# Optimization experiments

Measured on AMD Instinct MI355X. Metric: run time of the kernel, lower is better.

## Reference

```python
import jax, jax.numpy as jnp
import numpy as np

DIM = 128      # input node feature dim
GS = 64        # SAGEConv output dim
AF = 32        # additional (ir_score) feature dim
NB = 2         # nb_classes
G = 8192       # num_graphs in batch
NPG = 16       # nodes per graph
N = G * NPG    # total nodes = 131072
E = 2097152    # total edges (avg degree 16)


def setup_inputs() -> dict:
    key = jax.random.key(0)
    ks = jax.random.split(key, 10)

    def w(k, shape, fan_in):
        return jax.random.normal(k, shape, jnp.float32) / np.sqrt(fan_in)

    return {
        "x": jax.random.normal(ks[0], (N, DIM), jnp.float32),
        "edge_index": jax.random.randint(ks[1], (2, E), 0, N),
        "set_indices": jax.random.randint(ks[2], (G, 2), 0, NPG),
        "batch_ids": jnp.repeat(jnp.arange(G), NPG),  # sorted graph ids, PyG style
        "ir_score": jax.random.uniform(ks[3], (G, AF), jnp.float32),
        "W_l": w(ks[4], (DIM, GS), DIM),
        "b_l": jnp.zeros((GS,), jnp.float32),
        "W_r": w(ks[5], (DIM, GS), DIM),
        "W_ir": w(ks[6], (AF, 2 * GS), AF),
        "b_ir": jnp.zeros((2 * GS,), jnp.float32),
        "W1": w(ks[7], ((2 * GS) * (2 * GS), 200), (2 * GS) * (2 * GS)),
        "b1": jnp.zeros((200,), jnp.float32),
        "W2": w(ks[8], (200, NB), 200),
        "b2": jnp.zeros((NB,), jnp.float32),
    }


def reference(x, edge_index, set_indices, batch_ids, ir_score,
              W_l, b_l, W_r, W_ir, b_ir, W1, b1, W2, b2):
    n = x.shape[0]
    src, dst = edge_index[0], edge_index[1]

    # SAGEConv (mean aggregation): out = lin_l(mean_{j in N(i)} x_j) + lin_r(x_i)
    agg = jax.ops.segment_sum(x[src], dst, num_segments=n)           # [N, DIM]
    deg = jax.ops.segment_sum(jnp.ones((src.shape[0],), x.dtype), dst, num_segments=n)
    mean = agg / jnp.maximum(deg, 1.0)[:, None]
    h = jax.nn.relu(mean @ W_l + b_l + x @ W_r)                      # [N, GS]

    # per-graph node counts -> index bases (cumsum), then global pair indices
    g = set_indices.shape[0]
    num_nodes = jax.ops.segment_sum(jnp.ones((n,), jnp.float32), batch_ids, num_segments=g)
    csum = jnp.cumsum(num_nodes.astype(jnp.int64))
    index_bases = jnp.concatenate([jnp.zeros((1,), jnp.int64), csum[:-1]])
    sib = index_bases[:, None] + set_indices                         # [G, 2]

    pair = h[sib].reshape(g, 2 * GS)                                 # gather + flatten

    # fusion: relu(linear(ir_score)) then per-graph outer product
    S = jax.nn.relu(ir_score @ W_ir + b_ir)                          # [G, 2*GS]
    outer = jnp.einsum('gi,gj->gij', pair, S).reshape(g, -1)         # [G, (2GS)^2]

    # decode MLP
    z = jax.nn.relu(outer @ W1 + b1)                                 # [G, 200]
    logits = z @ W2 + b2                                             # [G, NB]
    return logits
```

## Files before the change

kernel.cpp:

```cpp
#include <hip/hip_runtime.h>

#define NN   131072
#define GG   8192
#define EE   2097152
#define KBIG 16384
#define NPAD 224
#define NSPLIT 8
#define NSEL  16384
#define SBUCK 256
#define SUBC  4
#define SCAPS 336
#define SCAPT (SUBC*SCAPS)

typedef _Float16 half_t;
typedef __attribute__((ext_vector_type(8))) _Float16 half8;
typedef __attribute__((ext_vector_type(4))) float floatx4;

__device__ inline floatx4 mfma16(half8 a, half8 b, floatx4 c) {
  return __builtin_amdgcn_mfma_f32_16x16x32_f16(a, b, c, 0, 0, 0);
}

__global__ void prep_w(const float* __restrict__ Wl, const float* __restrict__ Wr,
                       half_t* __restrict__ Wt) {
  int idx = blockIdx.x * blockDim.x + threadIdx.x;
  int n = idx >> 7, k = idx & 127;
  float v = (n < 64) ? Wl[k * 64 + n] : Wr[k * 64 + (n - 64)];
  Wt[n * 128 + k] = (half_t)v;
}
__global__ void prep_w1p(const float* __restrict__ W1, half_t* __restrict__ W1p) {
  int idx = blockIdx.x * blockDim.x + threadIdx.x;
  int lane = idx & 63;
  int t = idx >> 6;
  int nt = t % 14; t /= 14;
  int jc = t & 3;  t >>= 2;
  int i  = t & 15; t >>= 4;
  int split = t;
  int n = nt * 16 + (lane & 15);
  int k0 = split * 2048 + i * 128 + jc * 32 + (lane >> 4) * 8;
  half8 v;
#pragma unroll
  for (int e = 0; e < 8; e++)
    v[e] = (half_t)((n < 200) ? W1[(size_t)(k0 + e) * 200 + n] : 0.f);
  *(half8*)(W1p + (size_t)idx * 8) = v;
}

__global__ void set_slots(const int* __restrict__ set_idx, int* __restrict__ nodemap,
                          int* __restrict__ slot_node) {
  int idx = blockIdx.x * blockDim.x + threadIdx.x;
  int g = idx >> 1, which = idx & 1;
  int node = g * 16 + set_idx[g * 2 + which];
  slot_node[idx] = node;
  nodemap[node] = idx;
}

__global__ void filter_scatter(const int* __restrict__ src, const int* __restrict__ dst,
                               const int* __restrict__ nodemap,
                               int* __restrict__ scnt, unsigned int* __restrict__ sbuf) {
  int e = blockIdx.x * blockDim.x + threadIdx.x;
  int d = dst[e];
  int slot = nodemap[d];
  if (slot >= 0) {
    int b = slot >> 6;
    int sub = blockIdx.x & (SUBC - 1);
    int pos = atomicAdd(&scnt[(b * SUBC + sub) * 16], 1);
    if (pos < SCAPS)
      sbuf[(size_t)(b * SUBC + sub) * SCAPS + pos] =
          (unsigned int)src[e] | ((unsigned int)(slot & 63) << 17);
  }
}

__global__ __launch_bounds__(256) void y_gemm(const float* __restrict__ x,
                                              const half_t* __restrict__ WtG,
                                              half_t* __restrict__ y16) {
  __shared__ half_t wlds[64 * 128];
  __shared__ half_t ybuf[64 * 72];
  int tid = threadIdx.x, w = tid >> 6, lane = tid & 63;
  int m = lane & 15, q = lane >> 4, kc = q * 8;
#pragma unroll
  for (int it = 0; it < 4; it++) {
    int cb = (it * 4 + w) * 64;
    const half_t* g = WtG + ((size_t)cb + lane) * 8;
    half_t* l = wlds + (size_t)cb * 8;
    __builtin_amdgcn_global_load_lds((const __attribute__((address_space(1))) uint32_t*)g,
                                     (__attribute__((address_space(3))) uint32_t*)l, 16, 0, 0);
  }
  int node0 = blockIdx.x * 64 + w * 16;
  float4 xu[4][2];
#pragma unroll
  for (int step = 0; step < 4; step++) {
    const float* xp = x + (size_t)(node0 + m) * 128 + step * 32 + kc;
    xu[step][0] = *(const float4*)xp;
    xu[step][1] = *(const float4*)(xp + 4);
  }
  __syncthreads();
  floatx4 acc[4];
#pragma unroll
  for (int nt = 0; nt < 4; nt++) acc[nt] = (floatx4){0.f, 0.f, 0.f, 0.f};
#pragma unroll
  for (int step = 0; step < 4; step++) {
    float4 u0 = xu[step][0], u1 = xu[step][1];
    half8 av = {(half_t)u0.x, (half_t)u0.y, (half_t)u0.z, (half_t)u0.w,
                (half_t)u1.x, (half_t)u1.y, (half_t)u1.z, (half_t)u1.w};
    int k0 = step * 32 + kc;
#pragma unroll
    for (int nt = 0; nt < 4; nt++) {
      half8 bv = *(const half8*)(wlds + (nt * 16 + m) * 128 + k0);
      acc[nt] = mfma16(av, bv, acc[nt]);
    }
  }
#pragma unroll
  for (int nt = 0; nt < 4; nt++)
#pragma unroll
    for (int r = 0; r < 4; r++)
      ybuf[(w * 16 + q * 4 + r) * 72 + nt * 16 + m] = (half_t)acc[nt][r];
  __syncthreads();
#pragma unroll
  for (int c = tid; c < 512; c += 256) {
    int row = c >> 3, co = (c & 7) * 8;
    *(half8*)(y16 + (size_t)(blockIdx.x * 64 + row) * 64 + co) =
        *(const half8*)(ybuf + row * 72 + co);
  }
}

__global__ __launch_bounds__(256) void r_slots(const float* __restrict__ x,
                                               const half_t* __restrict__ WtG,
                                               const float* __restrict__ b_l,
                                               const int* __restrict__ slot_node,
                                               half_t* __restrict__ r_slot) {
  int tid = threadIdx.x, w = tid >> 6, lane = tid & 63;
  int m = lane & 15, q = lane >> 4, kc = q * 8;
  int s0 = blockIdx.x * 64 + w * 16;
  int node = slot_node[s0 + m];
  floatx4 acc[4];
#pragma unroll
  for (int nt = 0; nt < 4; nt++) acc[nt] = (floatx4){0.f, 0.f, 0.f, 0.f};
#pragma unroll
  for (int step = 0; step < 4; step++) {
    int k0 = step * 32 + kc;
    const float* xp = x + (size_t)node * 128 + k0;
    float4 u0 = *(const float4*)xp;
    float4 u1 = *(const float4*)(xp + 4);
    half8 av = {(half_t)u0.x, (half_t)u0.y, (half_t)u0.z, (half_t)u0.w,
                (half_t)u1.x, (half_t)u1.y, (half_t)u1.z, (half_t)u1.w};
#pragma unroll
    for (int nt = 0; nt < 4; nt++) {
      half8 bv = *(const half8*)(WtG + (size_t)(64 + nt * 16 + m) * 128 + k0);
      acc[nt] = mfma16(av, bv, acc[nt]);
    }
  }
#pragma unroll
  for (int nt = 0; nt < 4; nt++) {
    int n = nt * 16 + m;
    float bias = b_l[n];
#pragma unroll
    for (int r = 0; r < 4; r++) {
      int s = s0 + q * 4 + r;
      r_slot[(size_t)s * 64 + n] = (half_t)(acc[nt][r] + bias);
    }
  }
}

__global__ __launch_bounds__(256) void slot_agg(const unsigned int* __restrict__ sbuf,
                                                const int* __restrict__ scnt,
                                                const half_t* __restrict__ y16,
                                                const half_t* __restrict__ r_slot,
                                                half_t* __restrict__ h_slot) {
  __shared__ int sorted[SCAPT];
  __shared__ int hist[64];
  __shared__ int base[64];
  __shared__ int start[65];
  int b = blockIdx.x, tid = threadIdx.x;
  if (tid < 64) hist[tid] = 0;
  __syncthreads();
  unsigned int myedge[2 * SUBC];
  int mycnt = 0;
#pragma unroll
  for (int sub = 0; sub < SUBC; sub++) {
    int n = scnt[(b * SUBC + sub) * 16]; if (n > SCAPS) n = SCAPS;
    const unsigned int* eb = sbuf + (size_t)(b * SUBC + sub) * SCAPS;
    for (int e = tid; e < n; e += 256) {
      unsigned int pk = eb[e];
      myedge[mycnt++] = pk;
      atomicAdd(&hist[pk >> 17], 1);
    }
  }
  __syncthreads();
  if (tid < 64) {
    int v = hist[tid];
    int sum = v;
#pragma unroll
    for (int off = 1; off < 64; off <<= 1) {
      int u = __shfl_up(sum, off);
      if (tid >= off) sum += u;
    }
    start[tid] = sum - v;
    base[tid]  = sum - v;
    if (tid == 63) start[64] = sum;
  }
  __syncthreads();
  for (int i = 0; i < mycnt; i++) {
    unsigned int pk = myedge[i];
    int pos = atomicAdd(&base[pk >> 17], 1);
    sorted[pos] = (int)(pk & 0x1FFFF);
  }
  __syncthreads();
  int s = tid >> 2, p = tid & 3;
  int e0 = start[s], e1 = start[s + 1];
  float acc[16];
#pragma unroll
  for (int j = 0; j < 16; j++) acc[j] = 0.f;
  int e = e0;
  for (; e + 2 <= e1; e += 2) {
    int s0 = sorted[e], s1 = sorted[e + 1];
    const half8* p0 = (const half8*)(y16 + (size_t)s0 * 64 + p * 16);
    const half8* p1 = (const half8*)(y16 + (size_t)s1 * 64 + p * 16);
    half8 a0 = p0[0], c0 = p0[1], a1 = p1[0], c1 = p1[1];
#pragma unroll
    for (int j = 0; j < 8; j++) {
      acc[j]     += (float)a0[j] + (float)a1[j];
      acc[8 + j] += (float)c0[j] + (float)c1[j];
    }
  }
  if (e < e1) {
    int s0 = sorted[e];
    const half8* p0 = (const half8*)(y16 + (size_t)s0 * 64 + p * 16);
    half8 a0 = p0[0], c0 = p0[1];
#pragma unroll
    for (int j = 0; j < 8; j++) { acc[j] += (float)a0[j]; acc[8 + j] += (float)c0[j]; }
  }
  int slot = b * 64 + s;
  float inv = 1.0f / fmaxf((float)(e1 - e0), 1.0f);
  const half8* rr = (const half8*)(r_slot + (size_t)slot * 64 + p * 16);
  half8 r0 = rr[0], r1 = rr[1];
  half8 o0, o1;
#pragma unroll
  for (int j = 0; j < 8; j++) {
    o0[j] = (half_t)fmaxf(acc[j] * inv + (float)r0[j], 0.f);
    o1[j] = (half_t)fmaxf(acc[8 + j] * inv + (float)r1[j], 0.f);
  }
  half8* hp = (half8*)(h_slot + (size_t)slot * 64 + p * 16);
  hp[0] = o0;
  hp[1] = o1;
}

__global__ void s_pair_kernel(const float* __restrict__ ir, const float* __restrict__ W_ir,
                              const float* __restrict__ b_ir, half_t* __restrict__ S16,
                              const half_t* __restrict__ h_slot,
                              const int* __restrict__ nodemap,
                              const int* __restrict__ set_idx, half_t* __restrict__ pair16) {
  int idx = blockIdx.x * blockDim.x + threadIdx.x;
  int g = idx >> 7, o = idx & 127;
  const float* irow = ir + g * 32;
  float sv = b_ir[o];
#pragma unroll
  for (int a = 0; a < 32; a++) sv += irow[a] * W_ir[a * 128 + o];
  S16[idx] = (half_t)fmaxf(sv, 0.f);
  int which = o >> 6, c = o & 63;
  int node = g * 16 + set_idx[g * 2 + which];
  int slot = nodemap[node];
  pair16[idx] = h_slot[(size_t)slot * 64 + c];
}

__global__ __launch_bounds__(256, 2) void biggemm(const half_t* __restrict__ pair16,
                                                  const half_t* __restrict__ S16,
                                                  const half_t* __restrict__ W1p,
                                                  float* __restrict__ zpart) {
  __shared__ __align__(16) half_t bbuf[2][28 * 512];
  __shared__ half_t pls[16][128];
  int bx = blockIdx.x;
  int mt = bx >> 3, split = bx & 7;
  int g0 = mt * 128;
  int tid = threadIdx.x, w = tid >> 6, lane = tid & 63;
  int wm = w >> 1, wn = w & 1;
  int m = lane & 15, q = lane >> 4, kc = q * 8;
  int ntb = wn * 7;

  auto stage = [&](int ii, int halfsel, int bufsel) {
#pragma unroll
    for (int ff = 0; ff < 7; ff++) {
      int f = ff * 4 + w;
      const half_t* gsrc = W1p + (((size_t)(split * 16 + ii) * 56) + halfsel * 28 + f) * 512 + lane * 8;
      half_t* ldst = &bbuf[bufsel][f * 512];
      __builtin_amdgcn_global_load_lds((const __attribute__((address_space(1))) uint32_t*)gsrc,
                                       (__attribute__((address_space(3))) uint32_t*)ldst, 16, 0, 0);
    }
  };

  stage(0, 0, 0);

  {
    int row = tid & 127, sel = tid >> 7;
    half8 pa = *(const half8*)(pair16 + (size_t)(g0 + row) * 128 + split * 16 + sel * 8);
#pragma unroll
    for (int j = 0; j < 8; j++) pls[sel * 8 + j][row] = pa[j];
  }

  half8 sf[4][4];
#pragma unroll
  for (int sub = 0; sub < 4; sub++) {
    int grow = g0 + wm * 64 + sub * 16 + m;
#pragma unroll
    for (int jc = 0; jc < 4; jc++)
      sf[sub][jc] = *(const half8*)(S16 + (size_t)grow * 128 + jc * 32 + kc);
  }

  floatx4 acc[4][7];
#pragma unroll
  for (int sb = 0; sb < 4; sb++)
#pragma unroll
    for (int t = 0; t < 7; t++) acc[sb][t] = (floatx4){0.f, 0.f, 0.f, 0.f};

  for (int i = 0; i < 16; i++) {
    half_t p0, p1, p2, p3;
#pragma unroll
    for (int h2 = 0; h2 < 2; h2++) {
      __syncthreads();
      if (h2 == 0) {
        p0 = pls[i][wm * 64 + 0 * 16 + m];
        p1 = pls[i][wm * 64 + 1 * 16 + m];
        p2 = pls[i][wm * 64 + 2 * 16 + m];
        p3 = pls[i][wm * 64 + 3 * 16 + m];
        stage(i, 1, 1);
      } else if (i < 15) {
        stage(i + 1, 0, 0);
      }
      const half_t* bb = bbuf[h2];
#pragma unroll
      for (int jj = 0; jj < 2; jj++) {
        const int jc = h2 * 2 + jj;
        half8 a0 = sf[0][jc] * p0;
        half8 a1 = sf[1][jc] * p1;
        half8 a2 = sf[2][jc] * p2;
        half8 a3 = sf[3][jc] * p3;
#pragma unroll
        for (int t = 0; t < 7; t++) {
          half8 bv = *(const half8*)(bb + (jj * 14 + ntb + t) * 512 + lane * 8);
          acc[0][t] = mfma16(a0, bv, acc[0][t]);
          acc[1][t] = mfma16(a1, bv, acc[1][t]);
          acc[2][t] = mfma16(a2, bv, acc[2][t]);
          acc[3][t] = mfma16(a3, bv, acc[3][t]);
        }
      }
    }
  }

  float* ebuf = (float*)bbuf;
#pragma unroll
  for (int c = 0; c < 4; c++) {
    __syncthreads();
    if (wm == (c >> 1)) {
      int sb0 = (c & 1) * 2;
#pragma unroll
      for (int ss = 0; ss < 2; ss++) {
#pragma unroll
        for (int t = 0; t < 7; t++)
#pragma unroll
          for (int r = 0; r < 4; r++) {
            int lr = ss * 16 + q * 4 + r;
            ebuf[lr * 228 + (ntb + t) * 16 + m] = acc[sb0 + ss][t][r];
          }
      }
    }
    __syncthreads();
    int rbase = g0 + (c >> 1) * 64 + (c & 1) * 32;
#pragma unroll
    for (int u = tid; u < 1792; u += 256) {
      int lr = u / 56, co = (u % 56) * 4;
      *(float4*)(zpart + ((size_t)split * GG + rbase + lr) * NPAD + co) =
          *(const float4*)(ebuf + lr * 228 + co);
    }
  }
}

__global__ __launch_bounds__(256) void reduce_mlp(const float* __restrict__ zpart,
                                                  const float* __restrict__ b1,
                                                  const float* __restrict__ W2,
                                                  const float* __restrict__ b2,
                                                  float* __restrict__ out) {
  int tid = threadIdx.x;
  int w = tid >> 6, lane = tid & 63;
  int g = blockIdx.x * 4 + w;
  float p0 = 0.f, p1 = 0.f;
#pragma unroll
  for (int qq = 0; qq < 4; qq++) {
    int c = qq * 64 + lane;
    if (c < 200) {
      float z = 0.f;
#pragma unroll
      for (int sp = 0; sp < NSPLIT; sp++)
        z += zpart[((size_t)sp * GG + g) * NPAD + c];
      z += b1[c];
      z = fmaxf(z, 0.f);
      p0 += z * W2[c * 2];
      p1 += z * W2[c * 2 + 1];
    }
  }
#pragma unroll
  for (int off = 32; off; off >>= 1) {
    p0 += __shfl_down(p0, off);
    p1 += __shfl_down(p1, off);
  }
  if (lane == 0) {
    out[g * 2] = p0 + b2[0];
    out[g * 2 + 1] = p1 + b2[1];
  }
}

extern "C" void kernel_launch(void* const* d_in, const int* in_sizes, int n_in,
                              void* d_out, int out_size, void* d_ws, size_t ws_size,
                              hipStream_t stream) {
  const float* x     = (const float*)d_in[0];
  const int*   ei    = (const int*)d_in[1];
  const int*   setix = (const int*)d_in[2];
  const float* ir    = (const float*)d_in[4];
  const float* W_l   = (const float*)d_in[5];
  const float* b_l   = (const float*)d_in[6];
  const float* W_r   = (const float*)d_in[7];
  const float* W_ir  = (const float*)d_in[8];
  const float* b_ir  = (const float*)d_in[9];
  const float* W1    = (const float*)d_in[10];
  const float* b1    = (const float*)d_in[11];
  const float* W2    = (const float*)d_in[12];
  const float* b2    = (const float*)d_in[13];
  float* out = (float*)d_out;

  char* ws = (char*)d_ws;
  size_t off = 0;
  auto alloc = [&](size_t bytes) -> void* {
    void* p = ws + off;
    off = (off + bytes + 255) & ~(size_t)255;
    return p;
  };
  size_t pool_start = off;
  int* nodemap   = (int*)alloc((size_t)NN * 4);
  int* slot_node = (int*)alloc((size_t)NSEL * 4);
  int* scnt      = (int*)alloc((size_t)SBUCK * SUBC * 16 * 4);
  unsigned int* sbuf = (unsigned int*)alloc((size_t)SBUCK * SUBC * SCAPS * 4);
  half_t* y16    = (half_t*)alloc((size_t)NN * 64 * 2);
  half_t* r_slot = (half_t*)alloc((size_t)NSEL * 64 * 2);
  half_t* h_slot = (half_t*)alloc((size_t)NSEL * 64 * 2);
  float* zpart = (float*)(ws + pool_start);
  {
    size_t zend = pool_start + (((size_t)NSPLIT * GG * NPAD * 4 + 255) & ~(size_t)255);
    if (off < zend) off = zend;
  }
  half_t* Wt     = (half_t*)alloc(128 * 128 * 2);
  half_t* W1p    = (half_t*)alloc((size_t)NPAD * KBIG * 2);
  half_t* S16    = (half_t*)alloc((size_t)GG * 128 * 2);
  half_t* pair16 = (half_t*)alloc((size_t)GG * 128 * 2);
  (void)ws_size; (void)in_sizes; (void)n_in; (void)out_size;

  const int* esrc = ei;
  const int* edst = ei + EE;

  hipMemsetAsync(nodemap, 0xFF, (size_t)NN * 4, stream);
  hipMemsetAsync(scnt, 0, (size_t)SBUCK * SUBC * 16 * 4, stream);

  prep_w<<<(128 * 128) / 256, 256, 0, stream>>>(W_l, W_r, Wt);
  prep_w1p<<<(NPAD * KBIG / 8) / 256, 256, 0, stream>>>(W1, W1p);

  set_slots<<<NSEL / 256, 256, 0, stream>>>(setix, nodemap, slot_node);
  filter_scatter<<<EE / 256, 256, 0, stream>>>(esrc, edst, nodemap, scnt, sbuf);

  y_gemm<<<NN / 64, 256, 0, stream>>>(x, Wt, y16);
  r_slots<<<NSEL / 64, 256, 0, stream>>>(x, Wt, b_l, slot_node, r_slot);
  slot_agg<<<SBUCK, 256, 0, stream>>>(sbuf, scnt, y16, r_slot, h_slot);

  s_pair_kernel<<<(GG * 128) / 256, 256, 0, stream>>>(ir, W_ir, b_ir, S16, h_slot, nodemap, setix, pair16);

  biggemm<<<(GG / 128) * NSPLIT, 256, 0, stream>>>(pair16, S16, W1p, zpart);
  reduce_mlp<<<GG / 4, 256, 0, stream>>>(zpart, b1, W2, b2, out);
}
```

Measured before the change: 303.1 us.

## Reorder biggemm K loop into two S-halves to cut register use

Rearranges the packed W1 layout and the biggemm main loop so the K dimension is walked in two phases, each using half of the S columns. Each thread then holds half as many S fragments in registers. The loop becomes a single flat double-buffered stage per step, giving one barrier per step, and is fully unrolled. The epilogue now writes accumulators straight to global memory instead of staging them through LDS, which removes barriers but replaces coalesced float4 stores with scattered scalar stores.

```diff
diff --git a/kernel.cpp b/kernel.cpp
--- a/kernel.cpp
+++ b/kernel.cpp
@@ -32,11 +32,12 @@
   int lane = idx & 63;
   int t = idx >> 6;
   int nt = t % 14; t /= 14;
-  int jc = t & 3;  t >>= 2;
+  int jj = t & 1;  t >>= 1;
   int i  = t & 15; t >>= 4;
+  int ph = t & 1;  t >>= 1;
   int split = t;
   int n = nt * 16 + (lane & 15);
-  int k0 = split * 2048 + i * 128 + jc * 32 + (lane >> 4) * 8;
+  int k0 = split * 2048 + i * 128 + ph * 64 + jj * 32 + (lane >> 4) * 8;
   half8 v;
 #pragma unroll
   for (int e = 0; e < 8; e++)
@@ -275,12 +276,12 @@
   int m = lane & 15, q = lane >> 4, kc = q * 8;
   int ntb = wn * 7;
 
-  auto stage = [&](int ii, int halfsel, int bufsel) {
+  auto stage = [&](int ph, int ii, int buf) {
 #pragma unroll
     for (int ff = 0; ff < 7; ff++) {
       int f = ff * 4 + w;
-      const half_t* gsrc = W1p + (((size_t)(split * 16 + ii) * 56) + halfsel * 28 + f) * 512 + lane * 8;
-      half_t* ldst = &bbuf[bufsel][f * 512];
+      const half_t* gsrc = W1p + ((((size_t)(split * 2 + ph) * 16 + ii) * 28) + f) * 512 + lane * 8;
+      half_t* ldst = &bbuf[buf][f * 512];
       __builtin_amdgcn_global_load_lds((const __attribute__((address_space(1))) uint32_t*)gsrc,
                                        (__attribute__((address_space(3))) uint32_t*)ldst, 16, 0, 0);
     }
@@ -295,43 +296,42 @@
     for (int j = 0; j < 8; j++) pls[sel * 8 + j][row] = pa[j];
   }
 
-  half8 sf[4][4];
-#pragma unroll
-  for (int sub = 0; sub < 4; sub++) {
-    int grow = g0 + wm * 64 + sub * 16 + m;
-#pragma unroll
-    for (int jc = 0; jc < 4; jc++)
-      sf[sub][jc] = *(const half8*)(S16 + (size_t)grow * 128 + jc * 32 + kc);
-  }
-
   floatx4 acc[4][7];
 #pragma unroll
   for (int sb = 0; sb < 4; sb++)
 #pragma unroll
     for (int t = 0; t < 7; t++) acc[sb][t] = (floatx4){0.f, 0.f, 0.f, 0.f};
 
-  for (int i = 0; i < 16; i++) {
-    half_t p0, p1, p2, p3;
-#pragma unroll
-    for (int h2 = 0; h2 < 2; h2++) {
+  half8 sf[4][2];
+#pragma unroll
+  for (int ph = 0; ph < 2; ph++) {
+#pragma unroll
+    for (int sub = 0; sub < 4; sub++) {
+      int grow = g0 + wm * 64 + sub * 16 + m;
+#pragma unroll
+      for (int j2 = 0; j2 < 2; j2++)
+        sf[sub][j2] = *(const half8*)(S16 + (size_t)grow * 128 + ph * 64 + j2 * 32 + kc);
+    }
+#pragma unroll
+    for (int i = 0; i < 16; i++) {
+      int s = ph * 16 + i;
+      int cur = s & 1;
       __syncthreads();
-      if (h2 == 0) {
-        p0 = pls[i][wm * 64 + 0 * 16 + m];
-        p1 = pls[i][wm * 64 + 1 * 16 + m];
-        p2 = pls[i][wm * 64 + 2 * 16 + m];
-        p3 = pls[i][wm * 64 + 3 * 16 + m];
-        stage(i, 1, 1);
-      } else if (i < 15) {
-        stage(i + 1, 0, 0);
+      half_t p0 = pls[i][wm * 64 + 0 * 16 + m];
+      half_t p1 = pls[i][wm * 64 + 1 * 16 + m];
+      half_t p2 = pls[i][wm * 64 + 2 * 16 + m];
+      half_t p3 = pls[i][wm * 64 + 3 * 16 + m];
+      if (s < 31) {
+        int s1 = s + 1;
+        stage(s1 >> 4, s1 & 15, cur ^ 1);
       }
-      const half_t* bb = bbuf[h2];
+      const half_t* bb = bbuf[cur];
 #pragma unroll
       for (int jj = 0; jj < 2; jj++) {
-        const int jc = h2 * 2 + jj;
-        half8 a0 = sf[0][jc] * p0;
-        half8 a1 = sf[1][jc] * p1;
-        half8 a2 = sf[2][jc] * p2;
-        half8 a3 = sf[3][jc] * p3;
+        half8 a0 = sf[0][jj] * p0;
+        half8 a1 = sf[1][jj] * p1;
+        half8 a2 = sf[2][jj] * p2;
+        half8 a3 = sf[3][jj] * p3;
 #pragma unroll
         for (int t = 0; t < 7; t++) {
           half8 bv = *(const half8*)(bb + (jj * 14 + ntb + t) * 512 + lane * 8);
@@ -344,32 +344,15 @@
     }
   }
 
-  float* ebuf = (float*)bbuf;
-#pragma unroll
-  for (int c = 0; c < 4; c++) {
-    __syncthreads();
-    if (wm == (c >> 1)) {
-      int sb0 = (c & 1) * 2;
-#pragma unroll
-      for (int ss = 0; ss < 2; ss++) {
-#pragma unroll
-        for (int t = 0; t < 7; t++)
-#pragma unroll
-          for (int r = 0; r < 4; r++) {
-            int lr = ss * 16 + q * 4 + r;
-            ebuf[lr * 228 + (ntb + t) * 16 + m] = acc[sb0 + ss][t][r];
-          }
+#pragma unroll
+  for (int sub = 0; sub < 4; sub++)
+#pragma unroll
+    for (int t = 0; t < 7; t++)
+#pragma unroll
+      for (int r = 0; r < 4; r++) {
+        int row = g0 + wm * 64 + sub * 16 + q * 4 + r;
+        zpart[((size_t)split * GG + row) * NPAD + (ntb + t) * 16 + m] = acc[sub][t][r];
       }
-    }
-    __syncthreads();
-    int rbase = g0 + (c >> 1) * 64 + (c & 1) * 32;
-#pragma unroll
-    for (int u = tid; u < 1792; u += 256) {
-      int lr = u / 56, co = (u % 56) * 4;
-      *(float4*)(zpart + ((size_t)split * GG + rbase + lr) * NPAD + co) =
-          *(const float4*)(ebuf + lr * 228 + co);
-    }
-  }
 }
 
 __global__ __launch_bounds__(256) void reduce_mlp(const float* __restrict__ zpart,
```

Measured after the change: 260.2 us. -14.2%, faster.
